# Kernel tuning notes

Hardware: AMD Instinct MI355X
Metric: run time of the kernel (lower is better)

The kernel has to match this reference:

```python
import jax, jax.numpy as jnp
import numpy as np

N_HEADS = 16


def sparsemax(z):
    """Sparsemax along the last axis (Martins & Astudillo 2016)."""
    S = z.shape[-1]
    z_sorted = -jnp.sort(-z, axis=-1)                      # descending
    cs = jnp.cumsum(z_sorted, axis=-1)
    k = jnp.arange(1, S + 1, dtype=z.dtype)
    support = (1.0 + k * z_sorted) > cs                    # bool mask of support
    k_z = jnp.sum(support.astype(jnp.int32), axis=-1, keepdims=True)  # support size >=1
    cs_k = jnp.take_along_axis(cs, k_z - 1, axis=-1)
    tau = (cs_k - 1.0) / k_z.astype(z.dtype)
    return jnp.maximum(z - tau, 0.0)


def setup_inputs() -> dict:
    key = jax.random.key(0)
    ks = jax.random.split(key, 5)
    B, S, D = 4, 1024, 1024
    scale = 1.0 / np.sqrt(D).astype(np.float32)
    return {
        "x": jax.random.normal(ks[0], (B, S, D), jnp.float32),
        "Wq": jax.random.normal(ks[1], (D, D), jnp.float32) * scale,
        "bq": jnp.zeros((D,), jnp.float32),
        "Wk": jax.random.normal(ks[2], (D, D), jnp.float32) * scale,
        "bk": jnp.zeros((D,), jnp.float32),
        "Wv": jax.random.normal(ks[3], (D, D), jnp.float32) * scale,
        "bv": jnp.zeros((D,), jnp.float32),
        "Wo": jax.random.normal(ks[4], (D, D), jnp.float32) * scale,
        "bo": jnp.zeros((D,), jnp.float32),
    }


def reference(x, Wq, bq, Wk, bk, Wv, bv, Wo, bo):
    B, S, D = x.shape
    H = N_HEADS
    dh = D // H
    q = x @ Wq + bq                                        # (B,S,D)
    k = x @ Wk + bk
    v = x @ Wv + bv
    # split to heads: (B,H,S,dh)
    qh = q.reshape(B, S, H, dh).transpose(0, 2, 1, 3)
    kh = k.reshape(B, S, H, dh).transpose(0, 2, 1, 3)
    logits = jnp.einsum("bhqd,bhkd->bhqk", qh, kh) / np.sqrt(dh).astype(np.float32)
    probs = sparsemax(logits)                              # (B,H,S,S)
    # shared V: mean over head components, replicated per head
    v_shared = v.reshape(B, S, H, dh).mean(axis=2)         # (B,S,dh)
    out_h = jnp.einsum("bhqk,bkd->bhqd", probs, v_shared)  # (B,H,S,dh)
    x_out = out_h.transpose(0, 2, 1, 3).reshape(B, S, D) @ Wo + bo
    avg_attention = probs.mean(axis=1)                     # (B,S,S)
    return (x_out, avg_attention)
```

## Files before the change

### kernel.cpp

```cpp
#include <hip/hip_runtime.h>

#define B_  4
#define S_  1024
#define D_  1024
#define H_  16
#define DH  64
#define BS  4096

typedef __bf16 bf16x8 __attribute__((ext_vector_type(8)));
typedef float  f32x4  __attribute__((ext_vector_type(4)));

__device__ __forceinline__ unsigned short f2bf(float f) {
    __bf16 b = (__bf16)f;
    return __builtin_bit_cast(unsigned short, b);
}
__device__ __forceinline__ float bf2f(unsigned short u) {
    return (float)__builtin_bit_cast(__bf16, u);
}
__device__ __forceinline__ void glds16(const void* g, void* l) {
    __builtin_amdgcn_global_load_lds((const __attribute__((address_space(1))) void*)g,
                                     (__attribute__((address_space(3))) void*)l, 16, 0, 0);
}

__global__ __launch_bounds__(256) void prep2(const float* __restrict__ Wq,
                                             const float* __restrict__ Wk,
                                             const float* __restrict__ Wo,
                                             const float* __restrict__ Wv,
                                             const float* __restrict__ bv,
                                             const float* __restrict__ x,
                                             unsigned short* __restrict__ WqTh,
                                             unsigned short* __restrict__ WqTl,
                                             unsigned short* __restrict__ WkTh,
                                             unsigned short* __restrict__ WkTl,
                                             unsigned short* __restrict__ WoTh,
                                             unsigned short* __restrict__ WvTh,
                                             unsigned short* __restrict__ WvTl,
                                             float* __restrict__ bvp,
                                             float* __restrict__ avg,
                                             unsigned short* __restrict__ xh,
                                             unsigned short* __restrict__ xl) {
    __shared__ float tile[32][33];
    int bid = blockIdx.x, tid = threadIdx.x;
    if (bid < 3072) {
        const float* W;
        unsigned short *Th, *Tl;
        int wantLo;
        if (bid < 1024)      { W = Wq; Th = WqTh; Tl = WqTl; wantLo = 1; }
        else if (bid < 2048) { W = Wk; Th = WkTh; Tl = WkTl; wantLo = 1; bid -= 1024; }
        else                 { W = Wo; Th = WoTh; Tl = nullptr; wantLo = 0; bid -= 2048; }
        int tn = bid & 31, tk = bid >> 5;
        int r = tid >> 3, c4 = (tid & 7) * 4;
        float4 v = *(const float4*)(W + (size_t)(tk * 32 + r) * D_ + tn * 32 + c4);
        tile[r][c4 + 0] = v.x;
        tile[r][c4 + 1] = v.y;
        tile[r][c4 + 2] = v.z;
        tile[r][c4 + 3] = v.w;
        __syncthreads();
        unsigned short hh[4], ll[4];
#pragma unroll
        for (int i = 0; i < 4; i++) {
            float f = tile[c4 + i][r];
            hh[i] = f2bf(f);
            ll[i] = f2bf(f - bf2f(hh[i]));
        }
        size_t off = (size_t)(tn * 32 + r) * D_ + tk * 32 + c4;
        *(uint2*)(Th + off) = make_uint2((unsigned)hh[0] | ((unsigned)hh[1] << 16),
                                         (unsigned)hh[2] | ((unsigned)hh[3] << 16));
        if (wantLo)
            *(uint2*)(Tl + off) = make_uint2((unsigned)ll[0] | ((unsigned)ll[1] << 16),
                                             (unsigned)ll[2] | ((unsigned)ll[3] << 16));
    } else if (bid < 3328) {
        int e = (bid - 3072) * 256 + tid;
        int d = e >> 6, j = e & 63;
        float s = 0.f;
#pragma unroll
        for (int hh = 0; hh < H_; hh++) s += Wv[(size_t)d * D_ + hh * DH + j];
        s *= (1.f / 16.f);
        unsigned short hi = f2bf(s);
        WvTh[(size_t)j * D_ + d] = hi;
        WvTl[(size_t)j * D_ + d] = f2bf(s - bf2f(hi));
        if (bid == 3072 && tid < 128) {
            float sb = 0.f;
            if (tid < 64) {
#pragma unroll
                for (int hh = 0; hh < H_; hh++) sb += bv[hh * DH + tid];
                sb *= (1.f / 16.f);
            }
            bvp[tid] = sb;
        }
    } else if (bid < 3584) {
        int e = (bid - 3328) * 256 + tid;
        int row = 64 + (e >> 10), col = e & 1023;
        WvTh[(size_t)row * D_ + col] = 0;
        WvTl[(size_t)row * D_ + col] = 0;
    } else if (bid < 7680) {
        int e = (bid - 3584) * 256 + tid;
        *(float4*)(avg + (size_t)e * 4) = make_float4(0.f, 0.f, 0.f, 0.f);
    } else {
        size_t base = ((size_t)(bid - 7680) * 256 + tid) * 8;
        float4 f0 = *(const float4*)(x + base);
        float4 f1 = *(const float4*)(x + base + 4);
        float vv[8] = {f0.x, f0.y, f0.z, f0.w, f1.x, f1.y, f1.z, f1.w};
        unsigned hw[4], lw[4];
#pragma unroll
        for (int i = 0; i < 4; i++) {
            unsigned short h0 = f2bf(vv[2 * i]), h1 = f2bf(vv[2 * i + 1]);
            unsigned short l0 = f2bf(vv[2 * i] - bf2f(h0));
            unsigned short l1 = f2bf(vv[2 * i + 1] - bf2f(h1));
            hw[i] = (unsigned)h0 | ((unsigned)h1 << 16);
            lw[i] = (unsigned)l0 | ((unsigned)l1 << 16);
        }
        *(uint4*)(xh + base) = make_uint4(hw[0], hw[1], hw[2], hw[3]);
        *(uint4*)(xl + base) = make_uint4(lw[0], lw[1], lw[2], lw[3]);
    }
}

__global__ __launch_bounds__(256) void projg(const float* __restrict__ x,
                                             const unsigned short* __restrict__ WqTh, const unsigned short* __restrict__ WqTl,
                                             const unsigned short* __restrict__ WkTh, const unsigned short* __restrict__ WkTl,
                                             const unsigned short* __restrict__ WvTh, const unsigned short* __restrict__ WvTl,
                                             const float* __restrict__ bq, const float* __restrict__ bk,
                                             const float* __restrict__ bvp,
                                             unsigned short* __restrict__ qh, unsigned short* __restrict__ ql,
                                             unsigned short* __restrict__ kh, unsigned short* __restrict__ kl,
                                             float* __restrict__ vshb) {
    __shared__ unsigned short AhS[128 * 32];
    __shared__ unsigned short AlS[128 * 32];
    __shared__ unsigned short BhS[128 * 32];
    __shared__ unsigned short BlS[128 * 32];

    int tid = threadIdx.x, w = tid >> 6, lane = tid & 63;
    int m16 = lane & 15, qd = lane >> 4;
    int bn = blockIdx.x, bm = blockIdx.y;

    const unsigned short *Bh, *Bl;
    const float* bias;
    int mode;
    if (bn < 8)       { Bh = WqTh + (size_t)bn * 128 * D_;       Bl = WqTl + (size_t)bn * 128 * D_;       bias = bq + bn * 128;       mode = 0; }
    else if (bn < 16) { Bh = WkTh + (size_t)(bn - 8) * 128 * D_; Bl = WkTl + (size_t)(bn - 8) * 128 * D_; bias = bk + (bn - 8) * 128; mode = 1; }
    else              { Bh = WvTh; Bl = WvTl; bias = bvp; mode = 2; }

    int l4 = lane >> 2, c8 = (lane & 3) * 8;
    int rh = (w >> 1) * 64, chh = (w & 1) * 64;

    f32x4 acc[4][4];
#pragma unroll
    for (int it = 0; it < 4; it++)
#pragma unroll
        for (int jt = 0; jt < 4; jt++) acc[it][jt] = (f32x4){0.f, 0.f, 0.f, 0.f};

    int ra = tid >> 1, ca = (tid & 1) * 16;

    for (int k0 = 0; k0 < D_; k0 += 32) {
        const float* ax = x + (size_t)(bm * 128 + ra) * D_ + k0 + ca;
        float4 f0 = *(const float4*)(ax + 0);
        float4 f1 = *(const float4*)(ax + 4);
        float4 f2 = *(const float4*)(ax + 8);
        float4 f3 = *(const float4*)(ax + 12);
        __syncthreads();
        {
            float vv[16] = {f0.x, f0.y, f0.z, f0.w, f1.x, f1.y, f1.z, f1.w,
                            f2.x, f2.y, f2.z, f2.w, f3.x, f3.y, f3.z, f3.w};
            unsigned int hw[8], lw[8];
#pragma unroll
            for (int i = 0; i < 8; i++) {
                unsigned short h0 = f2bf(vv[2 * i]), h1 = f2bf(vv[2 * i + 1]);
                unsigned short l0 = f2bf(vv[2 * i] - bf2f(h0));
                unsigned short l1 = f2bf(vv[2 * i + 1] - bf2f(h1));
                hw[i] = (unsigned)h0 | ((unsigned)h1 << 16);
                lw[i] = (unsigned)l0 | ((unsigned)l1 << 16);
            }
            char* ah = (char*)AhS + ra * 64 + ca * 2;
            char* al = (char*)AlS + ra * 64 + ca * 2;
            *(uint4*)(ah + 0)  = make_uint4(hw[0], hw[1], hw[2], hw[3]);
            *(uint4*)(ah + 16) = make_uint4(hw[4], hw[5], hw[6], hw[7]);
            *(uint4*)(al + 0)  = make_uint4(lw[0], lw[1], lw[2], lw[3]);
            *(uint4*)(al + 16) = make_uint4(lw[4], lw[5], lw[6], lw[7]);
        }
        {
            const unsigned short* gbh = Bh + (size_t)(w * 32 + l4) * D_ + k0 + c8;
            const unsigned short* gbl = Bl + (size_t)(w * 32 + l4) * D_ + k0 + c8;
            glds16(gbh,                     (char*)BhS + w * 2048);
            glds16(gbh + (size_t)16 * D_,   (char*)BhS + w * 2048 + 1024);
            glds16(gbl,                     (char*)BlS + w * 2048);
            glds16(gbl + (size_t)16 * D_,   (char*)BlS + w * 2048 + 1024);
        }
        __syncthreads();
        bf16x8 ah[4], al[4], bh[4], bl[4];
#pragma unroll
        for (int it = 0; it < 4; it++) {
            ah[it] = *(const bf16x8*)((char*)AhS + (rh + it * 16 + m16) * 64 + qd * 16);
            al[it] = *(const bf16x8*)((char*)AlS + (rh + it * 16 + m16) * 64 + qd * 16);
        }
#pragma unroll
        for (int jt = 0; jt < 4; jt++) {
            bh[jt] = *(const bf16x8*)((char*)BhS + (chh + jt * 16 + m16) * 64 + qd * 16);
            bl[jt] = *(const bf16x8*)((char*)BlS + (chh + jt * 16 + m16) * 64 + qd * 16);
        }
#pragma unroll
        for (int it = 0; it < 4; it++)
#pragma unroll
            for (int jt = 0; jt < 4; jt++) {
                acc[it][jt] = __builtin_amdgcn_mfma_f32_16x16x32_bf16(ah[it], bh[jt], acc[it][jt], 0, 0, 0);
                acc[it][jt] = __builtin_amdgcn_mfma_f32_16x16x32_bf16(ah[it], bl[jt], acc[it][jt], 0, 0, 0);
                acc[it][jt] = __builtin_amdgcn_mfma_f32_16x16x32_bf16(al[it], bh[jt], acc[it][jt], 0, 0, 0);
            }
    }
#pragma unroll
    for (int it = 0; it < 4; it++)
#pragma unroll
        for (int jt = 0; jt < 4; jt++)
#pragma unroll
            for (int r = 0; r < 4; r++) {
                int R = bm * 128 + rh + it * 16 + qd * 4 + r;
                int c = chh + jt * 16 + m16;
                float v = acc[it][jt][r] + bias[c];
                if (mode == 0) {
                    v *= 0.125f;
                    unsigned short h0 = f2bf(v);
                    qh[(size_t)R * D_ + bn * 128 + c] = h0;
                    ql[(size_t)R * D_ + bn * 128 + c] = f2bf(v - bf2f(h0));
                } else if (mode == 1) {
                    unsigned short h0 = f2bf(v);
                    kh[(size_t)R * D_ + (bn - 8) * 128 + c] = h0;
                    kl[(size_t)R * D_ + (bn - 8) * 128 + c] = f2bf(v - bf2f(h0));
                } else {
                    if (c < 64) vshb[(size_t)R * 64 + c] = v;
                }
            }
}

__global__ __launch_bounds__(256) void projgx(const unsigned short* __restrict__ xh,
                                              const unsigned short* __restrict__ xl,
                                              const unsigned short* __restrict__ WqTh, const unsigned short* __restrict__ WqTl,
                                              const unsigned short* __restrict__ WkTh, const unsigned short* __restrict__ WkTl,
                                              const unsigned short* __restrict__ WvTh, const unsigned short* __restrict__ WvTl,
                                              const float* __restrict__ bq, const float* __restrict__ bk,
                                              const float* __restrict__ bvp,
                                              unsigned short* __restrict__ qh, unsigned short* __restrict__ ql,
                                              unsigned short* __restrict__ kh, unsigned short* __restrict__ kl,
                                              float* __restrict__ vshb) {
    __shared__ unsigned short AhS[64 * 32];
    __shared__ unsigned short AlS[64 * 32];
    __shared__ unsigned short BhS[128 * 32];
    __shared__ unsigned short BlS[128 * 32];

    int tid = threadIdx.x, w = tid >> 6, lane = tid & 63;
    int m16 = lane & 15, qd = lane >> 4;
    int bn = blockIdx.x, bm = blockIdx.y;

    const unsigned short *Bh, *Bl;
    const float* bias;
    int mode;
    if (bn < 8)       { Bh = WqTh + (size_t)bn * 128 * D_;       Bl = WqTl + (size_t)bn * 128 * D_;       bias = bq + bn * 128;       mode = 0; }
    else if (bn < 16) { Bh = WkTh + (size_t)(bn - 8) * 128 * D_; Bl = WkTl + (size_t)(bn - 8) * 128 * D_; bias = bk + (bn - 8) * 128; mode = 1; }
    else              { Bh = WvTh; Bl = WvTl; bias = bvp; mode = 2; }

    int l4 = lane >> 2, c8 = (lane & 3) * 8;
    int rh = (w >> 1) * 32, chh = (w & 1) * 64;

    f32x4 acc[2][4];
#pragma unroll
    for (int it = 0; it < 2; it++)
#pragma unroll
        for (int jt = 0; jt < 4; jt++) acc[it][jt] = (f32x4){0.f, 0.f, 0.f, 0.f};

    for (int k0 = 0; k0 < D_; k0 += 32) {
        __syncthreads();
        {
            const unsigned short* gah = xh + (size_t)(bm * 64 + w * 16 + l4) * D_ + k0 + c8;
            const unsigned short* gal = xl + (size_t)(bm * 64 + w * 16 + l4) * D_ + k0 + c8;
            glds16(gah, (char*)AhS + w * 1024);
            glds16(gal, (char*)AlS + w * 1024);
            const unsigned short* gbh = Bh + (size_t)(w * 32 + l4) * D_ + k0 + c8;
            const unsigned short* gbl = Bl + (size_t)(w * 32 + l4) * D_ + k0 + c8;
            glds16(gbh,                     (char*)BhS + w * 2048);
            glds16(gbh + (size_t)16 * D_,   (char*)BhS + w * 2048 + 1024);
            glds16(gbl,                     (char*)BlS + w * 2048);
            glds16(gbl + (size_t)16 * D_,   (char*)BlS + w * 2048 + 1024);
        }
        __syncthreads();
        bf16x8 ah[2], al[2], bh[4], bl[4];
#pragma unroll
        for (int it = 0; it < 2; it++) {
            ah[it] = *(const bf16x8*)((char*)AhS + (rh + it * 16 + m16) * 64 + qd * 16);
            al[it] = *(const bf16x8*)((char*)AlS + (rh + it * 16 + m16) * 64 + qd * 16);
        }
#pragma unroll
        for (int jt = 0; jt < 4; jt++) {
            bh[jt] = *(const bf16x8*)((char*)BhS + (chh + jt * 16 + m16) * 64 + qd * 16);
            bl[jt] = *(const bf16x8*)((char*)BlS + (chh + jt * 16 + m16) * 64 + qd * 16);
        }
#pragma unroll
        for (int it = 0; it < 2; it++)
#pragma unroll
            for (int jt = 0; jt < 4; jt++) {
                acc[it][jt] = __builtin_amdgcn_mfma_f32_16x16x32_bf16(ah[it], bh[jt], acc[it][jt], 0, 0, 0);
                acc[it][jt] = __builtin_amdgcn_mfma_f32_16x16x32_bf16(ah[it], bl[jt], acc[it][jt], 0, 0, 0);
                acc[it][jt] = __builtin_amdgcn_mfma_f32_16x16x32_bf16(al[it], bh[jt], acc[it][jt], 0, 0, 0);
            }
    }
#pragma unroll
    for (int it = 0; it < 2; it++)
#pragma unroll
        for (int jt = 0; jt < 4; jt++)
#pragma unroll
            for (int r = 0; r < 4; r++) {
                int R = bm * 64 + rh + it * 16 + qd * 4 + r;
                int c = chh + jt * 16 + m16;
                float v = acc[it][jt][r] + bias[c];
                if (mode == 0) {
                    v *= 0.125f;
                    unsigned short h0 = f2bf(v);
                    qh[(size_t)R * D_ + bn * 128 + c] = h0;
                    ql[(size_t)R * D_ + bn * 128 + c] = f2bf(v - bf2f(h0));
                } else if (mode == 1) {
                    unsigned short h0 = f2bf(v);
                    kh[(size_t)R * D_ + (bn - 8) * 128 + c] = h0;
                    kl[(size_t)R * D_ + (bn - 8) * 128 + c] = f2bf(v - bf2f(h0));
                } else {
                    if (c < 64) vshb[(size_t)R * 64 + c] = v;
                }
            }
}

__global__ __launch_bounds__(256) void outg(const unsigned short* __restrict__ A,
                                            const unsigned short* __restrict__ Bh,
                                            const float* __restrict__ bias,
                                            float* __restrict__ C) {
    __shared__ unsigned short AhS[64 * 32];
    __shared__ unsigned short BhS[64 * 32];

    int tid = threadIdx.x, w = tid >> 6, lane = tid & 63;
    int m16 = lane & 15, qd = lane >> 4;
    int bn = blockIdx.x, bm = blockIdx.y;
    int l4 = lane >> 2, c8 = (lane & 3) * 8;
    int rh = (w >> 1) * 32, chh = (w & 1) * 32;

    f32x4 acc[2][2];
#pragma unroll
    for (int it = 0; it < 2; it++)
#pragma unroll
        for (int jt = 0; jt < 2; jt++) acc[it][jt] = (f32x4){0.f, 0.f, 0.f, 0.f};

    for (int k0 = 0; k0 < D_; k0 += 32) {
        __syncthreads();
        {
            const unsigned short* ga = A + (size_t)(bm * 64 + w * 16 + l4) * D_ + k0 + c8;
            glds16(ga, (char*)AhS + w * 1024);
            const unsigned short* gb = Bh + (size_t)(bn * 64 + w * 16 + l4) * D_ + k0 + c8;
            glds16(gb, (char*)BhS + w * 1024);
        }
        __syncthreads();
        bf16x8 ah[2], bh[2];
#pragma unroll
        for (int it = 0; it < 2; it++)
            ah[it] = *(const bf16x8*)((char*)AhS + (rh + it * 16 + m16) * 64 + qd * 16);
#pragma unroll
        for (int jt = 0; jt < 2; jt++)
            bh[jt] = *(const bf16x8*)((char*)BhS + (chh + jt * 16 + m16) * 64 + qd * 16);
#pragma unroll
        for (int it = 0; it < 2; it++)
#pragma unroll
            for (int jt = 0; jt < 2; jt++)
                acc[it][jt] = __builtin_amdgcn_mfma_f32_16x16x32_bf16(ah[it], bh[jt], acc[it][jt], 0, 0, 0);
    }
#pragma unroll
    for (int it = 0; it < 2; it++)
#pragma unroll
        for (int jt = 0; jt < 2; jt++)
#pragma unroll
            for (int r = 0; r < 4; r++) {
                int R = bm * 64 + rh + it * 16 + qd * 4 + r;
                int cc = bn * 64 + chh + jt * 16 + m16;
                C[(size_t)R * D_ + cc] = acc[it][jt][r] + bias[cc];
            }
}

#define CCAP 48
__global__ __launch_bounds__(256, 4) void attn8(const unsigned short* __restrict__ qh,
                                                const unsigned short* __restrict__ ql,
                                                const unsigned short* __restrict__ kh,
                                                const unsigned short* __restrict__ kl,
                                                const float* __restrict__ vsh,
                                                unsigned short* __restrict__ och,
                                                float* __restrict__ avg) {
    __shared__ __align__(16) char KST[32768];
    __shared__ float smM[4][16];
    __shared__ float smS[4][16], smC[4][16];
    __shared__ float tau0s[16];
    __shared__ float taus[16];
    __shared__ int   ccnt[16];
    __shared__ int   ovfAny;
    __shared__ int   scnt16[16];

    float (*candV)[CCAP] = (float (*)[CCAP])(KST);
    short (*candI)[CCAP] = (short (*)[CCAP])(KST + 3072);
    float (*slotV)[16]   = (float (*)[16])(KST + 4608);
    short (*slotI)[16]   = (short (*)[16])(KST + 5632);

    int tid = threadIdx.x, w = tid >> 6, lane = tid & 63;
    int m16 = lane & 15, qd = lane >> 4;

    int bid = blockIdx.x;
    int xcd = bid & 7;
    int j   = bid >> 3;
    int bh  = ((j >> 6) << 3) | xcd;
    int qt  = j & 63;
    int bb  = bh >> 4, h = bh & 15;
    int row0g = bb * S_ + qt * 16;
    int kbase = bb * S_;

    bf16x8 aH[2], aL[2];
#pragma unroll
    for (int c = 0; c < 2; c++) {
        size_t off = (size_t)(row0g + m16) * D_ + h * DH + c * 32 + qd * 8;
        aH[c] = *(const bf16x8*)(qh + off);
        aL[c] = *(const bf16x8*)(ql + off);
    }

    f32x4 Cfr[16];
#pragma unroll
    for (int t = 0; t < 16; t++) Cfr[t] = (f32x4){0.f, 0.f, 0.f, 0.f};

    char* myK = KST + w * 8192;
    {
        int sr = lane >> 3;
        int sc = (lane & 7) ^ sr;
        const unsigned short* ksh = kh + (size_t)(kbase + w * 256 + sr) * D_ + h * DH + sc * 8;
        const unsigned short* ksl = kl + (size_t)(kbase + w * 256 + sr) * D_ + h * DH + sc * 8;

#define STAGE_K(t, buf) do {                                        \
        size_t o_ = (size_t)(t) * 16 * D_;                          \
        char* db_ = myK + (buf) * 4096;                             \
        glds16(ksh + o_,                  db_);                     \
        glds16(ksh + o_ + (size_t)8 * D_, db_ + 1024);              \
        glds16(ksl + o_,                  db_ + 2048);              \
        glds16(ksl + o_ + (size_t)8 * D_, db_ + 3072);              \
    } while (0)

        int sw0 = m16 * 128 + (((qd    ) ^ (m16 & 7)) << 4);
        int sw1 = m16 * 128 + (((4 + qd) ^ (m16 & 7)) << 4);

        STAGE_K(0, 0);
        STAGE_K(1, 1);

#pragma unroll
        for (int t = 0; t < 16; t++) {
            if (t < 15) {
                asm volatile("s_waitcnt vmcnt(4)" ::: "memory");
            } else {
                asm volatile("s_waitcnt vmcnt(0)" ::: "memory");
            }
            __builtin_amdgcn_sched_barrier(0);
            const char* tbuf = myK + (t & 1) * 4096;
            bf16x8 bfh0 = *(const bf16x8*)(tbuf + sw0);
            bf16x8 bfh1 = *(const bf16x8*)(tbuf + sw1);
            bf16x8 bfl0 = *(const bf16x8*)(tbuf + 2048 + sw0);
            bf16x8 bfl1 = *(const bf16x8*)(tbuf + 2048 + sw1);
            asm volatile("s_waitcnt lgkmcnt(0)" ::: "memory");
            __builtin_amdgcn_sched_barrier(0);
            if (t + 2 <= 15) STAGE_K(t + 2, t & 1);
            f32x4 a = Cfr[t];
            __builtin_amdgcn_s_setprio(1);
            a = __builtin_amdgcn_mfma_f32_16x16x32_bf16(aH[0], bfh0, a, 0, 0, 0);
            a = __builtin_amdgcn_mfma_f32_16x16x32_bf16(aH[1], bfh1, a, 0, 0, 0);
            a = __builtin_amdgcn_mfma_f32_16x16x32_bf16(aH[0], bfl0, a, 0, 0, 0);
            a = __builtin_amdgcn_mfma_f32_16x16x32_bf16(aH[1], bfl1, a, 0, 0, 0);
            a = __builtin_amdgcn_mfma_f32_16x16x32_bf16(aL[0], bfh0, a, 0, 0, 0);
            a = __builtin_amdgcn_mfma_f32_16x16x32_bf16(aL[1], bfh1, a, 0, 0, 0);
            __builtin_amdgcn_s_setprio(0);
            Cfr[t] = a;
        }
#undef STAGE_K
    }

    float mxr[4];
#pragma unroll
    for (int r = 0; r < 4; r++) mxr[r] = -3.0e38f;
#pragma unroll
    for (int t = 0; t < 16; t++)
#pragma unroll
        for (int r = 0; r < 4; r++) mxr[r] = fmaxf(mxr[r], Cfr[t][r]);
#pragma unroll
    for (int off = 8; off >= 1; off >>= 1)
#pragma unroll
        for (int r = 0; r < 4; r++) mxr[r] = fmaxf(mxr[r], __shfl_xor(mxr[r], off, 16));
    if (m16 == 0)
#pragma unroll
        for (int r = 0; r < 4; r++) smM[w][qd * 4 + r] = mxr[r];
    if (tid < 16) ccnt[tid] = 0;
    if (tid == 0) ovfAny = 0;
    __syncthreads();
    if (tid < 16)
        tau0s[tid] = fmaxf(fmaxf(smM[0][tid], smM[1][tid]), fmaxf(smM[2][tid], smM[3][tid])) - 1.0f;
    __syncthreads();

    float t0r[4];
#pragma unroll
    for (int r = 0; r < 4; r++) t0r[r] = tau0s[qd * 4 + r];

#pragma unroll
    for (int t = 0; t < 16; t++)
#pragma unroll
        for (int r = 0; r < 4; r++) {
            float z = Cfr[t][r];
            int row = qd * 4 + r;
            if (z > t0r[r]) {
                int pos = atomicAdd(&ccnt[row], 1);
                if (pos < CCAP) {
                    candV[row][pos] = z;
                    candI[row][pos] = (short)(w * 256 + t * 16 + m16);
                }
            }
        }
    __syncthreads();
    if (tid < 16 && ccnt[tid] > CCAP) ovfAny = 1;

    int prow = tid >> 4, pc = tid & 15;
    int nc = ccnt[prow];
    float tau = tau0s[prow];
    float z0 = -3.0e38f, z1 = -3.0e38f, z2 = -3.0e38f;
    if (nc <= CCAP) {
        z0 = (pc < nc)      ? candV[prow][pc]      : -3.0e38f;
        z1 = (pc + 16 < nc) ? candV[prow][pc + 16] : -3.0e38f;
        z2 = (pc + 32 < nc) ? candV[prow][pc + 32] : -3.0e38f;
        for (int it = 0; it < CCAP; it++) {
            float s = 0.f, c = 0.f;
            if (z0 > tau) { s += z0; c += 1.f; }
            if (z1 > tau) { s += z1; c += 1.f; }
            if (z2 > tau) { s += z2; c += 1.f; }
#pragma unroll
            for (int off = 8; off >= 1; off >>= 1) {
                s += __shfl_xor(s, off, 16);
                c += __shfl_xor(c, off, 16);
            }
            float tnew = (s - 1.f) / c;
            if (tnew > tau) tau = tnew; else break;
        }
    }
    if (pc == 0) taus[prow] = tau;
    if (tid < 16) scnt16[tid] = 0;
    __syncthreads();

    if (!ovfAny) {
        if (z0 > tau) {
            int sl = atomicAdd(&scnt16[prow], 1);
            if (sl < 16) { slotI[prow][sl] = candI[prow][pc]; slotV[prow][sl] = z0 - tau; }
        }
        if (z1 > tau) {
            int sl = atomicAdd(&scnt16[prow], 1);
            if (sl < 16) { slotI[prow][sl] = candI[prow][pc + 16]; slotV[prow][sl] = z1 - tau; }
        }
        if (z2 > tau) {
            int sl = atomicAdd(&scnt16[prow], 1);
            if (sl < 16) { slotI[prow][sl] = candI[prow][pc + 32]; slotV[prow][sl] = z2 - tau; }
        }
        __syncthreads();
    } else {
        for (int it = 0; it < 64; it++) {
            float s[4], c[4];
#pragma unroll
            for (int r = 0; r < 4; r++) { s[r] = 0.f; c[r] = 0.f; }
#pragma unroll
            for (int t = 0; t < 16; t++)
#pragma unroll
                for (int r = 0; r < 4; r++) {
                    float z = Cfr[t][r];
                    if (z > taus[qd * 4 + r]) { s[r] += z; c[r] += 1.f; }
                }
#pragma unroll
            for (int off = 8; off >= 1; off >>= 1)
#pragma unroll
                for (int r = 0; r < 4; r++) {
                    s[r] += __shfl_xor(s[r], off, 16);
                    c[r] += __shfl_xor(c[r], off, 16);
                }
            if (m16 == 0)
#pragma unroll
                for (int r = 0; r < 4; r++) {
                    smS[w][qd * 4 + r] = s[r];
                    smC[w][qd * 4 + r] = c[r];
                }
            __syncthreads();
            int done = 1;
            if (tid < 16) {
                float S = smS[0][tid] + smS[1][tid] + smS[2][tid] + smS[3][tid];
                float C = smC[0][tid] + smC[1][tid] + smC[2][tid] + smC[3][tid];
                float tnew = (S - 1.f) / C;
                if (C > 0.f && tnew > taus[tid]) { taus[tid] = tnew; done = 0; }
            }
            if (__syncthreads_and(done)) break;
        }
#pragma unroll
        for (int t = 0; t < 16; t++)
#pragma unroll
            for (int r = 0; r < 4; r++) {
                int row = qd * 4 + r;
                float p = Cfr[t][r] - taus[row];
                if (p > 0.f) {
                    int sl = atomicAdd(&scnt16[row], 1);
                    if (sl < 16) {
                        slotI[row][sl] = (short)(w * 256 + t * 16 + m16);
                        slotV[row][sl] = p;
                    }
                }
            }
        __syncthreads();
    }

    int nsl = min(scnt16[prow], 16);
    f32x4 v0 = *(const f32x4*)&slotV[prow][0];
    f32x4 v1 = *(const f32x4*)&slotV[prow][4];
    f32x4 v2 = *(const f32x4*)&slotV[prow][8];
    f32x4 v3 = *(const f32x4*)&slotV[prow][12];
    const uint4* sIv = (const uint4*)&slotI[prow][0];
    uint4 i0 = sIv[0], i1 = sIv[1];
    float pA[16] = {v0[0], v0[1], v0[2], v0[3], v1[0], v1[1], v1[2], v1[3],
                    v2[0], v2[1], v2[2], v2[3], v3[0], v3[1], v3[2], v3[3]};
    unsigned wI[8] = {i0.x, i0.y, i0.z, i0.w, i1.x, i1.y, i1.z, i1.w};
    float4 accq = make_float4(0.f, 0.f, 0.f, 0.f);
#pragma unroll
    for (int sl = 0; sl < 16; sl++) {
        float p = (sl < nsl) ? pA[sl] : 0.f;
        int key = (int)((wI[sl >> 1] >> ((sl & 1) * 16)) & 1023u);
        float4 vv = *(const float4*)(vsh + (size_t)(kbase + key) * DH + pc * 4);
        accq.x += p * vv.x;
        accq.y += p * vv.y;
        accq.z += p * vv.z;
        accq.w += p * vv.w;
    }
    {
        unsigned short b0 = f2bf(accq.x), b1 = f2bf(accq.y), b2 = f2bf(accq.z), b3 = f2bf(accq.w);
        *(uint2*)(och + (size_t)(row0g + prow) * D_ + h * DH + pc * 4) =
            make_uint2((unsigned)b0 | ((unsigned)b1 << 16), (unsigned)b2 | ((unsigned)b3 << 16));
    }
    if (pc < nsl) {
        int key = (int)((wI[pc >> 1] >> ((pc & 1) * 16)) & 1023u);
        atomicAdd(avg + (size_t)(row0g + prow) * S_ + key, pA[pc] * 0.0625f);
    }
}

extern "C" void kernel_launch(void* const* d_in, const int* in_sizes, int n_in,
                              void* d_out, int out_size, void* d_ws, size_t ws_size,
                              hipStream_t stream) {
    const float* x  = (const float*)d_in[0];
    const float* Wq = (const float*)d_in[1];
    const float* bq = (const float*)d_in[2];
    const float* Wk = (const float*)d_in[3];
    const float* bk = (const float*)d_in[4];
    const float* Wv = (const float*)d_in[5];
    const float* bv = (const float*)d_in[6];
    const float* Wo = (const float*)d_in[7];
    const float* bo = (const float*)d_in[8];

    float* xout = (float*)d_out;
    float* avg  = xout + (size_t)BS * D_;

    char* ws = (char*)d_ws;
    unsigned short* qhB  = (unsigned short*)(ws + 0);
    unsigned short* qlB  = (unsigned short*)(ws + (8u << 20));
    unsigned short* khB  = (unsigned short*)(ws + (16u << 20));
    unsigned short* klB  = (unsigned short*)(ws + (24u << 20));
    unsigned short* WqTh = (unsigned short*)(ws + (32u << 20));
    unsigned short* WqTl = (unsigned short*)(ws + (34u << 20));
    unsigned short* WkTh = (unsigned short*)(ws + (36u << 20));
    unsigned short* WkTl = (unsigned short*)(ws + (38u << 20));
    unsigned short* ochB = WqTh;
    unsigned short* WoTh = (unsigned short*)(ws + (40u << 20));
    unsigned short* WvTh = (unsigned short*)(ws + (42u << 20));
    unsigned short* WvTl = (unsigned short*)(ws + (42u << 20) + (256u << 10));
    float* bvp = (float*)(ws + (42u << 20) + (512u << 10));
    float* vshb = (float*)(ws + (43u << 20));
    unsigned short* xhB = (unsigned short*)(ws + (44u << 20));
    unsigned short* xlB = (unsigned short*)(ws + (52u << 20));

    int bigws = ws_size >= ((size_t)60u << 20);

    prep2<<<bigws ? 9728 : 7680, 256, 0, stream>>>(Wq, Wk, Wo, Wv, bv, x,
                                                   WqTh, WqTl, WkTh, WkTl, WoTh, WvTh, WvTl,
                                                   bvp, avg, xhB, xlB);
    if (bigws) {
        projgx<<<dim3(17, 64), 256, 0, stream>>>(xhB, xlB, WqTh, WqTl, WkTh, WkTl, WvTh, WvTl,
                                                 bq, bk, bvp, qhB, qlB, khB, klB, vshb);
    } else {
        projg<<<dim3(17, 32), 256, 0, stream>>>(x, WqTh, WqTl, WkTh, WkTl, WvTh, WvTl,
                                                bq, bk, bvp, qhB, qlB, khB, klB, vshb);
    }
    attn8<<<4096, 256, 0, stream>>>(qhB, qlB, khB, klB, vshb, ochB, avg);
    outg<<<dim3(16, 64), 256, 0, stream>>>(ochB, WoTh, bo, xout);
}
```

Measured before the change: 336.3 us.

## Double-buffer weight tiles and load activation fragments directly in QKV projection GEMM

The projection GEMM now double-buffers the B (weight hi/lo) tiles in LDS and issues the next tile's global-to-LDS loads before computing on the current one, with explicit waitcnt and barriers. The A operand (x hi/lo) is no longer staged through LDS; each wave loads its MFMA fragments straight from global memory into registers and prefetches one step ahead. The goal is to hide global-load latency behind the MFMAs and cut LDS traffic, at the cost of more registers, fully unrolled code, and strided, less-coalesced A reads. Hand-placed vmcnt counts make correctness depend on the exact number of outstanding loads.

```diff
diff --git a/kernel.cpp b/kernel.cpp
--- a/kernel.cpp
+++ b/kernel.cpp
@@ -240,10 +240,8 @@
                                               unsigned short* __restrict__ qh, unsigned short* __restrict__ ql,
                                               unsigned short* __restrict__ kh, unsigned short* __restrict__ kl,
                                               float* __restrict__ vshb) {
-    __shared__ unsigned short AhS[64 * 32];
-    __shared__ unsigned short AlS[64 * 32];
-    __shared__ unsigned short BhS[128 * 32];
-    __shared__ unsigned short BlS[128 * 32];
+    __shared__ unsigned short BhS[2][128 * 32];
+    __shared__ unsigned short BlS[2][128 * 32];
 
     int tid = threadIdx.x, w = tid >> 6, lane = tid & 63;
     int m16 = lane & 15, qd = lane >> 4;
@@ -265,41 +263,70 @@
 #pragma unroll
         for (int jt = 0; jt < 4; jt++) acc[it][jt] = (f32x4){0.f, 0.f, 0.f, 0.f};
 
-    for (int k0 = 0; k0 < D_; k0 += 32) {
-        __syncthreads();
-        {
-            const unsigned short* gah = xh + (size_t)(bm * 64 + w * 16 + l4) * D_ + k0 + c8;
-            const unsigned short* gal = xl + (size_t)(bm * 64 + w * 16 + l4) * D_ + k0 + c8;
-            glds16(gah, (char*)AhS + w * 1024);
-            glds16(gal, (char*)AlS + w * 1024);
-            const unsigned short* gbh = Bh + (size_t)(w * 32 + l4) * D_ + k0 + c8;
-            const unsigned short* gbl = Bl + (size_t)(w * 32 + l4) * D_ + k0 + c8;
-            glds16(gbh,                     (char*)BhS + w * 2048);
-            glds16(gbh + (size_t)16 * D_,   (char*)BhS + w * 2048 + 1024);
-            glds16(gbl,                     (char*)BlS + w * 2048);
-            glds16(gbl + (size_t)16 * D_,   (char*)BlS + w * 2048 + 1024);
-        }
-        __syncthreads();
-        bf16x8 ah[2], al[2], bh[4], bl[4];
-#pragma unroll
-        for (int it = 0; it < 2; it++) {
-            ah[it] = *(const bf16x8*)((char*)AhS + (rh + it * 16 + m16) * 64 + qd * 16);
-            al[it] = *(const bf16x8*)((char*)AlS + (rh + it * 16 + m16) * 64 + qd * 16);
-        }
+    const unsigned short* a0h = xh + (size_t)(bm * 64 + rh + m16) * D_ + qd * 8;
+    const unsigned short* a1h = xh + (size_t)(bm * 64 + rh + 16 + m16) * D_ + qd * 8;
+    const unsigned short* a0l = xl + (size_t)(bm * 64 + rh + m16) * D_ + qd * 8;
+    const unsigned short* a1l = xl + (size_t)(bm * 64 + rh + 16 + m16) * D_ + qd * 8;
+
+#define STAGE_B(k0_, buf_) do {                                              \
+        const unsigned short* gbh = Bh + (size_t)(w * 32 + l4) * D_ + (k0_) + c8; \
+        const unsigned short* gbl = Bl + (size_t)(w * 32 + l4) * D_ + (k0_) + c8; \
+        glds16(gbh,                   (char*)BhS[buf_] + w * 2048);          \
+        glds16(gbh + (size_t)16 * D_, (char*)BhS[buf_] + w * 2048 + 1024);   \
+        glds16(gbl,                   (char*)BlS[buf_] + w * 2048);          \
+        glds16(gbl + (size_t)16 * D_, (char*)BlS[buf_] + w * 2048 + 1024);   \
+    } while (0)
+
+    bf16x8 ahC0 = *(const bf16x8*)(a0h);
+    bf16x8 ahC1 = *(const bf16x8*)(a1h);
+    bf16x8 alC0 = *(const bf16x8*)(a0l);
+    bf16x8 alC1 = *(const bf16x8*)(a1l);
+    STAGE_B(0, 0);
+    asm volatile("s_waitcnt vmcnt(0)" ::: "memory");
+    __builtin_amdgcn_s_barrier();
+    __builtin_amdgcn_sched_barrier(0);
+
+#pragma unroll
+    for (int k = 0; k < 32; k++) {
+        int cur = k & 1, nxt = cur ^ 1;
+        __builtin_amdgcn_s_barrier();
+        __builtin_amdgcn_sched_barrier(0);
+        bf16x8 ahN0, ahN1, alN0, alN1;
+        if (k < 31) {
+            int kn = (k + 1) * 32;
+            ahN0 = *(const bf16x8*)(a0h + kn);
+            ahN1 = *(const bf16x8*)(a1h + kn);
+            alN0 = *(const bf16x8*)(a0l + kn);
+            alN1 = *(const bf16x8*)(a1l + kn);
+            STAGE_B(kn, nxt);
+            asm volatile("s_waitcnt vmcnt(8)" ::: "memory");
+        } else {
+            asm volatile("s_waitcnt vmcnt(0)" ::: "memory");
+        }
+        __builtin_amdgcn_sched_barrier(0);
+        __builtin_amdgcn_s_barrier();
+        __builtin_amdgcn_sched_barrier(0);
+        bf16x8 bh[4], bl[4];
 #pragma unroll
         for (int jt = 0; jt < 4; jt++) {
-            bh[jt] = *(const bf16x8*)((char*)BhS + (chh + jt * 16 + m16) * 64 + qd * 16);
-            bl[jt] = *(const bf16x8*)((char*)BlS + (chh + jt * 16 + m16) * 64 + qd * 16);
-        }
-#pragma unroll
-        for (int it = 0; it < 2; it++)
-#pragma unroll
-            for (int jt = 0; jt < 4; jt++) {
-                acc[it][jt] = __builtin_amdgcn_mfma_f32_16x16x32_bf16(ah[it], bh[jt], acc[it][jt], 0, 0, 0);
-                acc[it][jt] = __builtin_amdgcn_mfma_f32_16x16x32_bf16(ah[it], bl[jt], acc[it][jt], 0, 0, 0);
-                acc[it][jt] = __builtin_amdgcn_mfma_f32_16x16x32_bf16(al[it], bh[jt], acc[it][jt], 0, 0, 0);
-            }
-    }
+            bh[jt] = *(const bf16x8*)((char*)BhS[cur] + (chh + jt * 16 + m16) * 64 + qd * 16);
+            bl[jt] = *(const bf16x8*)((char*)BlS[cur] + (chh + jt * 16 + m16) * 64 + qd * 16);
+        }
+        asm volatile("s_waitcnt lgkmcnt(0)" ::: "memory");
+        __builtin_amdgcn_sched_barrier(0);
+#pragma unroll
+        for (int jt = 0; jt < 4; jt++) {
+            acc[0][jt] = __builtin_amdgcn_mfma_f32_16x16x32_bf16(ahC0, bh[jt], acc[0][jt], 0, 0, 0);
+            acc[0][jt] = __builtin_amdgcn_mfma_f32_16x16x32_bf16(ahC0, bl[jt], acc[0][jt], 0, 0, 0);
+            acc[0][jt] = __builtin_amdgcn_mfma_f32_16x16x32_bf16(alC0, bh[jt], acc[0][jt], 0, 0, 0);
+            acc[1][jt] = __builtin_amdgcn_mfma_f32_16x16x32_bf16(ahC1, bh[jt], acc[1][jt], 0, 0, 0);
+            acc[1][jt] = __builtin_amdgcn_mfma_f32_16x16x32_bf16(ahC1, bl[jt], acc[1][jt], 0, 0, 0);
+            acc[1][jt] = __builtin_amdgcn_mfma_f32_16x16x32_bf16(alC1, bh[jt], acc[1][jt], 0, 0, 0);
+        }
+        if (k < 31) { ahC0 = ahN0; ahC1 = ahN1; alC0 = alN0; alC1 = alN1; }
+    }
+#undef STAGE_B
+
 #pragma unroll
     for (int it = 0; it < 2; it++)
 #pragma unroll
```

Result: slower. 365.1 us (+8.5%).
